# Kernel tuning notes

Measured on AMD Instinct MI355X. Metric: run time of the kernel, lower is better.

## Reference

```python
import jax, jax.numpy as jnp
import numpy as np

E = 64          # num_experts
D_IN = 512      # in_features
D_OUT = 512     # out_features
T = 262144      # total routed token-slots (grouped by expert, balanced)


def setup_inputs() -> dict:
    key = jax.random.key(0)
    k1, k2 = jax.random.split(key)
    STD = 0.02
    return {
        "input": jax.random.normal(k1, (T, D_IN), dtype=jnp.float32),
        # tokens are pre-grouped by expert; balanced routing -> equal counts
        "num_experts_per_token": jnp.full((E,), T // E, dtype=jnp.int64),
        "weight": jax.random.normal(k2, (E, D_OUT, D_IN), dtype=jnp.float32) * STD,
        "bias": jnp.zeros((E, D_OUT), dtype=jnp.float32),
    }


def reference(input, num_experts_per_token, weight, bias):
    # Faithful to the split + per-expert F.linear + cat path, for balanced
    # routing (equal counts per expert) so shapes are static under jit.
    e = weight.shape[0]
    tpe = input.shape[0] // e  # tokens per expert
    x = input.reshape(e, tpe, -1)                      # [E, tpe, D_in]
    # F.linear(x_e, W_e) = x_e @ W_e.T for each expert -> grouped GEMM
    out = jnp.einsum('eti,eoi->eto', x, weight)        # [E, tpe, D_out]
    out = out + bias[:, None, :]
    return out.reshape(e * tpe, -1)                    # [T, D_out]
```

## Files before the change

### kernel.cpp

```cpp
#include <hip/hip_runtime.h>
#include <hip/hip_bf16.h>


#define NEXPERT 64
#define DIN 512
#define DOUT 512
#define TPE 4096
#define BM 128
#define BN 256
#define BK 32
#define NKT (DIN / BK)

typedef __attribute__((ext_vector_type(8))) __bf16 bf16x8;
typedef __attribute__((ext_vector_type(4))) __bf16 bf16x4;
typedef __attribute__((ext_vector_type(4))) float f32x4;

__global__ __launch_bounds__(256)
void convert_w_kernel(const float* __restrict__ w, __bf16* __restrict__ wb) {
  size_t i = ((size_t)blockIdx.x * 256 + threadIdx.x) * 8;
  f32x4 a = *(const f32x4*)(w + i);
  f32x4 b = *(const f32x4*)(w + i + 4);
  bf16x8 r;
  r[0] = (__bf16)a[0]; r[1] = (__bf16)a[1]; r[2] = (__bf16)a[2]; r[3] = (__bf16)a[3];
  r[4] = (__bf16)b[0]; r[5] = (__bf16)b[1]; r[6] = (__bf16)b[2]; r[7] = (__bf16)b[3];
  *(bf16x8*)(wb + i) = r;
}

template <bool WB16>
__global__ __launch_bounds__(256, 2)
void moe_gemm(const float* __restrict__ x, const void* __restrict__ wsrc,
              const float* __restrict__ bias, float* __restrict__ out) {
  __shared__ __align__(16) unsigned char sA[2][BM * BK * 2];

  int bid = blockIdx.x;
  int swzb = (bid & 7) * 512 + (bid >> 3);
  int e  = swzb >> 6;
  int rr = swzb & 63;
  int mt = rr >> 1;
  int nt = rr & 1;

  const int tid  = threadIdx.x;
  const int lane = tid & 63;
  const int wn   = tid >> 6;
  const int r15  = lane & 15;
  const int kg   = lane >> 4;

  const int c4 = tid & 7;
  const int tr = tid >> 3;
  const float* aG = x + ((size_t)e * TPE + (size_t)mt * BM + tr) * DIN + c4 * 4;
  const int wrBase = tr * 64 + (((c4 >> 1) ^ ((tr >> 1) & 3)) << 4) + (c4 & 1) * 8;

  const int chz = (kg ^ ((r15 >> 1) & 3)) << 4;
  const int aRd = r15 * 64 + chz;

  const size_t bRow = (size_t)(e * DOUT + nt * BN + wn * 64 + r15) * DIN + kg * 8;
  const __bf16* bPb = (const __bf16*)wsrc + bRow;
  const float*  bPf = (const float*)wsrc + bRow;

  f32x4 sa0[4], sa1[4];
  bf16x8 b0v[4], b1v[4];

#define ISSUEA(kt, Sr)                                                      \
  { _Pragma("unroll") for (int i = 0; i < 4; ++i)                           \
      Sr[i] = *(const f32x4*)(aG + (size_t)i * 32 * DIN + (kt) * BK); }

#define WRITEA(dbuf, Sr)                                                    \
  { _Pragma("unroll") for (int i = 0; i < 4; ++i) {                         \
      bf16x4 c;                                                             \
      c[0] = (__bf16)Sr[i][0]; c[1] = (__bf16)Sr[i][1];                     \
      c[2] = (__bf16)Sr[i][2]; c[3] = (__bf16)Sr[i][3];                     \
      *(bf16x4*)(&sA[dbuf][wrBase + i * 2048]) = c; } }

#define LOADB(kt, Br)                                                       \
  { if constexpr (WB16) {                                                   \
      _Pragma("unroll") for (int n = 0; n < 4; ++n)                         \
        Br[n] = *(const bf16x8*)(bPb + (size_t)n * 16 * DIN + (kt) * BK);   \
    } else {                                                                \
      _Pragma("unroll") for (int n = 0; n < 4; ++n) {                       \
        f32x4 lo = *(const f32x4*)(bPf + (size_t)n * 16 * DIN + (kt) * BK); \
        f32x4 hi = *(const f32x4*)(bPf + (size_t)n * 16 * DIN + (kt) * BK + 4); \
        bf16x8 rv;                                                          \
        rv[0]=(__bf16)lo[0]; rv[1]=(__bf16)lo[1]; rv[2]=(__bf16)lo[2]; rv[3]=(__bf16)lo[3]; \
        rv[4]=(__bf16)hi[0]; rv[5]=(__bf16)hi[1]; rv[6]=(__bf16)hi[2]; rv[7]=(__bf16)hi[3]; \
        Br[n] = rv; } } }

#define MFMAS(Bv)                                                           \
  { _Pragma("unroll") for (int mi = 0; mi < 8; ++mi)                        \
      _Pragma("unroll") for (int ni = 0; ni < 4; ++ni)                      \
        acc[mi][ni] = __builtin_amdgcn_mfma_f32_16x16x32_bf16(              \
            af[mi], Bv[ni], acc[mi][ni], 0, 0, 0); }

  f32x4 acc[8][4];
#pragma unroll
  for (int m = 0; m < 8; ++m)
#pragma unroll
    for (int n = 0; n < 4; ++n) acc[m][n] = (f32x4)0.f;

  ISSUEA(0, sa0);
  ISSUEA(1, sa1);
  LOADB(0, b0v);
  WRITEA(0, sa0);
  asm volatile("s_waitcnt lgkmcnt(0)" ::: "memory");
  __builtin_amdgcn_s_barrier();

#pragma unroll
  for (int t = 0; t < NKT; ++t) {
    const int d = t & 1;
    bf16x8 af[8];
#pragma unroll
    for (int mi = 0; mi < 8; ++mi)
      af[mi] = *(const bf16x8*)(&sA[d][aRd + mi * 1024]);

    if (d == 0) {
      if (t + 1 < NKT) LOADB(t + 1, b1v);
      if (t + 2 < NKT) ISSUEA(t + 2, sa0);
      if (t + 1 < NKT) WRITEA(1, sa1);
      __builtin_amdgcn_s_setprio(1);
      MFMAS(b0v);
      __builtin_amdgcn_s_setprio(0);
    } else {
      if (t + 1 < NKT) LOADB(t + 1, b0v);
      if (t + 2 < NKT) ISSUEA(t + 2, sa1);
      if (t + 1 < NKT) WRITEA(0, sa0);
      __builtin_amdgcn_s_setprio(1);
      MFMAS(b1v);
      __builtin_amdgcn_s_setprio(0);
    }

    if (t + 1 < NKT) {
      asm volatile("s_waitcnt lgkmcnt(0)" ::: "memory");
      __builtin_amdgcn_s_barrier();
    }
  }

  float bv[4];
  const float* bp = bias + (size_t)e * DOUT + nt * BN + wn * 64 + r15;
#pragma unroll
  for (int n = 0; n < 4; ++n) bv[n] = bp[n * 16];

  const int q4 = (lane >> 4) * 4;
  float* Cb = out + ((size_t)e * TPE + (size_t)mt * BM) * DOUT + nt * BN + wn * 64;
#pragma unroll
  for (int m = 0; m < 8; ++m) {
#pragma unroll
    for (int j = 0; j < 4; ++j) {
      float* pr = Cb + (size_t)(m * 16 + q4 + j) * DOUT;
#pragma unroll
      for (int n = 0; n < 4; ++n)
        pr[n * 16 + r15] = acc[m][n][j] + bv[n];
    }
  }
#undef ISSUEA
#undef WRITEA
#undef LOADB
#undef MFMAS
}

extern "C" void kernel_launch(void* const* d_in, const int* in_sizes, int n_in,
                              void* d_out, int out_size, void* d_ws, size_t ws_size,
                              hipStream_t stream) {
  const float* x    = (const float*)d_in[0];
  const float* w    = (const float*)d_in[2];
  const float* bias = (const float*)d_in[3];
  float* out        = (float*)d_out;

  const size_t wElems = (size_t)NEXPERT * DOUT * DIN;
  const size_t needWs = wElems * sizeof(__hip_bfloat16);
  dim3 grid(NEXPERT * (TPE / BM) * (DOUT / BN));
  dim3 block(256);

  if (ws_size >= needWs) {
    dim3 cgrid(wElems / 8 / 256);
    hipLaunchKernelGGL(convert_w_kernel, cgrid, block, 0, stream,
                       w, (__bf16*)d_ws);
    hipLaunchKernelGGL(moe_gemm<true>, grid, block, 0, stream,
                       x, (const void*)d_ws, bias, out);
  } else {
    hipLaunchKernelGGL(moe_gemm<false>, grid, block, 0, stream,
                       x, (const void*)w, bias, out);
  }
}
```

Before: 339.6 us.

## Stage pre-packed bf16 weights into LDS via direct global-to-LDS loads

```diff
diff --git a/kernel.cpp b/kernel.cpp
--- a/kernel.cpp
+++ b/kernel.cpp
@@ -9,28 +9,36 @@
 #define BM 128
 #define BN 256
 #define BK 32
-#define NKT (DIN / BK)
+#define NKT 16
 
 typedef __attribute__((ext_vector_type(8))) __bf16 bf16x8;
 typedef __attribute__((ext_vector_type(4))) __bf16 bf16x4;
 typedef __attribute__((ext_vector_type(4))) float f32x4;
 
 __global__ __launch_bounds__(256)
-void convert_w_kernel(const float* __restrict__ w, __bf16* __restrict__ wb) {
-  size_t i = ((size_t)blockIdx.x * 256 + threadIdx.x) * 8;
-  f32x4 a = *(const f32x4*)(w + i);
-  f32x4 b = *(const f32x4*)(w + i + 4);
+void pack_w_kernel(const float* __restrict__ w, __bf16* __restrict__ wp) {
+  int S = blockIdx.x * 256 + threadIdx.x;
+  int l  = S & 63;
+  int c  = (S >> 6) & 15;
+  int kt = (S >> 10) & 15;
+  int nt = (S >> 14) & 1;
+  int e  = S >> 15;
+  int o  = nt * 256 + c * 16 + (l >> 2);
+  int kg = (l & 3) ^ ((l >> 3) & 3);
+  const float* src = w + ((size_t)(e * DOUT + o)) * DIN + kt * BK + kg * 8;
+  f32x4 lo = *(const f32x4*)(src);
+  f32x4 hi = *(const f32x4*)(src + 4);
   bf16x8 r;
-  r[0] = (__bf16)a[0]; r[1] = (__bf16)a[1]; r[2] = (__bf16)a[2]; r[3] = (__bf16)a[3];
-  r[4] = (__bf16)b[0]; r[5] = (__bf16)b[1]; r[6] = (__bf16)b[2]; r[7] = (__bf16)b[3];
-  *(bf16x8*)(wb + i) = r;
-}
-
-template <bool WB16>
+  r[0]=(__bf16)lo[0]; r[1]=(__bf16)lo[1]; r[2]=(__bf16)lo[2]; r[3]=(__bf16)lo[3];
+  r[4]=(__bf16)hi[0]; r[5]=(__bf16)hi[1]; r[6]=(__bf16)hi[2]; r[7]=(__bf16)hi[3];
+  *(bf16x8*)(wp + (size_t)S * 8) = r;
+}
+
 __global__ __launch_bounds__(256, 2)
-void moe_gemm(const float* __restrict__ x, const void* __restrict__ wsrc,
-              const float* __restrict__ bias, float* __restrict__ out) {
+void moe_gemm8(const float* __restrict__ x, const __bf16* __restrict__ wp,
+               const float* __restrict__ bias, float* __restrict__ out) {
   __shared__ __align__(16) unsigned char sA[2][BM * BK * 2];
+  __shared__ __align__(16) unsigned char sB[2][BN * BK * 2];
 
   int bid = blockIdx.x;
   int swzb = (bid & 7) * 512 + (bid >> 3);
@@ -52,43 +60,31 @@
 
   const int chz = (kg ^ ((r15 >> 1) & 3)) << 4;
   const int aRd = r15 * 64 + chz;
-
-  const size_t bRow = (size_t)(e * DOUT + nt * BN + wn * 64 + r15) * DIN + kg * 8;
-  const __bf16* bPb = (const __bf16*)wsrc + bRow;
-  const float*  bPf = (const float*)wsrc + bRow;
+  const int bRd = (wn * 64 + r15) * 64 + chz;
+
+  const __bf16* bSrc =
+      wp + ((size_t)(((e * 2 + nt) * 16) * 16 + wn * 4) * 64 + lane) * 8;
 
   f32x4 sa0[4], sa1[4];
-  bf16x8 b0v[4], b1v[4];
-
-#define ISSUEA(kt, Sr)                                                      \
-  { _Pragma("unroll") for (int i = 0; i < 4; ++i)                           \
+
+#define GLOADB(kt, dbuf)                                                     \
+  { _Pragma("unroll") for (int i = 0; i < 4; ++i)                            \
+      __builtin_amdgcn_global_load_lds(                                      \
+          (const __attribute__((address_space(1))) void*)(bSrc +             \
+              (size_t)(kt) * 8192 + i * 512),                                \
+          (__attribute__((address_space(3))) void*)(&sB[dbuf][(wn * 4 + i) * 1024]), \
+          16, 0, 0); }
+
+#define ISSUEA(kt, Sr)                                                       \
+  { _Pragma("unroll") for (int i = 0; i < 4; ++i)                            \
       Sr[i] = *(const f32x4*)(aG + (size_t)i * 32 * DIN + (kt) * BK); }
 
-#define WRITEA(dbuf, Sr)                                                    \
-  { _Pragma("unroll") for (int i = 0; i < 4; ++i) {                         \
-      bf16x4 c;                                                             \
-      c[0] = (__bf16)Sr[i][0]; c[1] = (__bf16)Sr[i][1];                     \
-      c[2] = (__bf16)Sr[i][2]; c[3] = (__bf16)Sr[i][3];                     \
-      *(bf16x4*)(&sA[dbuf][wrBase + i * 2048]) = c; } }
-
-#define LOADB(kt, Br)                                                       \
-  { if constexpr (WB16) {                                                   \
-      _Pragma("unroll") for (int n = 0; n < 4; ++n)                         \
-        Br[n] = *(const bf16x8*)(bPb + (size_t)n * 16 * DIN + (kt) * BK);   \
-    } else {                                                                \
-      _Pragma("unroll") for (int n = 0; n < 4; ++n) {                       \
-        f32x4 lo = *(const f32x4*)(bPf + (size_t)n * 16 * DIN + (kt) * BK); \
-        f32x4 hi = *(const f32x4*)(bPf + (size_t)n * 16 * DIN + (kt) * BK + 4); \
-        bf16x8 rv;                                                          \
-        rv[0]=(__bf16)lo[0]; rv[1]=(__bf16)lo[1]; rv[2]=(__bf16)lo[2]; rv[3]=(__bf16)lo[3]; \
-        rv[4]=(__bf16)hi[0]; rv[5]=(__bf16)hi[1]; rv[6]=(__bf16)hi[2]; rv[7]=(__bf16)hi[3]; \
-        Br[n] = rv; } } }
-
-#define MFMAS(Bv)                                                           \
-  { _Pragma("unroll") for (int mi = 0; mi < 8; ++mi)                        \
-      _Pragma("unroll") for (int ni = 0; ni < 4; ++ni)                      \
-        acc[mi][ni] = __builtin_amdgcn_mfma_f32_16x16x32_bf16(              \
-            af[mi], Bv[ni], acc[mi][ni], 0, 0, 0); }
+#define WRITEA(dbuf, Sr)                                                     \
+  { _Pragma("unroll") for (int i = 0; i < 4; ++i) {                          \
+      bf16x4 cc;                                                             \
+      cc[0] = (__bf16)Sr[i][0]; cc[1] = (__bf16)Sr[i][1];                    \
+      cc[2] = (__bf16)Sr[i][2]; cc[3] = (__bf16)Sr[i][3];                    \
+      *(bf16x4*)(&sA[dbuf][wrBase + i * 2048]) = cc; } }
 
   f32x4 acc[8][4];
 #pragma unroll
@@ -96,9 +92,9 @@
 #pragma unroll
     for (int n = 0; n < 4; ++n) acc[m][n] = (f32x4)0.f;
 
+  GLOADB(0, 0);
   ISSUEA(0, sa0);
   ISSUEA(1, sa1);
-  LOADB(0, b0v);
   WRITEA(0, sa0);
   asm volatile("s_waitcnt lgkmcnt(0)" ::: "memory");
   __builtin_amdgcn_s_barrier();
@@ -106,26 +102,47 @@
 #pragma unroll
   for (int t = 0; t < NKT; ++t) {
     const int d = t & 1;
-    bf16x8 af[8];
-#pragma unroll
-    for (int mi = 0; mi < 8; ++mi)
+    if (t == NKT - 1) {
+      asm volatile("s_waitcnt vmcnt(0)" ::: "memory");
+    } else {
+      asm volatile("s_waitcnt vmcnt(4)" ::: "memory");
+    }
+    if (t + 1 < NKT) GLOADB(t + 1, d ^ 1);
+    bf16x8 bfr[4], af[8];
+#pragma unroll
+    for (int ni = 0; ni < 4; ++ni)
+      bfr[ni] = *(const bf16x8*)(&sB[d][bRd + ni * 1024]);
+#pragma unroll
+    for (int mi = 0; mi < 4; ++mi)
       af[mi] = *(const bf16x8*)(&sA[d][aRd + mi * 1024]);
 
-    if (d == 0) {
-      if (t + 1 < NKT) LOADB(t + 1, b1v);
-      if (t + 2 < NKT) ISSUEA(t + 2, sa0);
-      if (t + 1 < NKT) WRITEA(1, sa1);
-      __builtin_amdgcn_s_setprio(1);
-      MFMAS(b0v);
-      __builtin_amdgcn_s_setprio(0);
-    } else {
-      if (t + 1 < NKT) LOADB(t + 1, b0v);
-      if (t + 2 < NKT) ISSUEA(t + 2, sa1);
-      if (t + 1 < NKT) WRITEA(0, sa0);
-      __builtin_amdgcn_s_setprio(1);
-      MFMAS(b1v);
-      __builtin_amdgcn_s_setprio(0);
-    }
+    if (t + 2 < NKT) {
+      if (d == 0) ISSUEA(t + 2, sa0) else ISSUEA(t + 2, sa1)
+    }
+    __builtin_amdgcn_s_setprio(1);
+#pragma unroll
+    for (int mi = 0; mi < 4; ++mi)
+#pragma unroll
+      for (int ni = 0; ni < 4; ++ni)
+        acc[mi][ni] = __builtin_amdgcn_mfma_f32_16x16x32_bf16(
+            af[mi], bfr[ni], acc[mi][ni], 0, 0, 0);
+    __builtin_amdgcn_s_setprio(0);
+
+#pragma unroll
+    for (int mi = 4; mi < 8; ++mi)
+      af[mi] = *(const bf16x8*)(&sA[d][aRd + mi * 1024]);
+    if (t + 1 < NKT) {
+      if (d == 0) WRITEA(1, sa1) else WRITEA(0, sa0)
+    }
+
+    __builtin_amdgcn_s_setprio(1);
+#pragma unroll
+    for (int mi = 4; mi < 8; ++mi)
+#pragma unroll
+      for (int ni = 0; ni < 4; ++ni)
+        acc[mi][ni] = __builtin_amdgcn_mfma_f32_16x16x32_bf16(
+            af[mi], bfr[ni], acc[mi][ni], 0, 0, 0);
+    __builtin_amdgcn_s_setprio(0);
 
     if (t + 1 < NKT) {
       asm volatile("s_waitcnt lgkmcnt(0)" ::: "memory");
@@ -150,10 +167,86 @@
         pr[n * 16 + r15] = acc[m][n][j] + bv[n];
     }
   }
+#undef GLOADB
 #undef ISSUEA
 #undef WRITEA
-#undef LOADB
-#undef MFMAS
+}
+
+typedef __attribute__((ext_vector_type(8))) __bf16 bf16x8_t;
+
+__device__ __forceinline__ bf16x8 cvt8f(f32x4 lo, f32x4 hi) {
+  bf16x8 r;
+  r[0]=(__bf16)lo[0]; r[1]=(__bf16)lo[1]; r[2]=(__bf16)lo[2]; r[3]=(__bf16)lo[3];
+  r[4]=(__bf16)hi[0]; r[5]=(__bf16)hi[1]; r[6]=(__bf16)hi[2]; r[7]=(__bf16)hi[3];
+  return r;
+}
+
+__global__ __launch_bounds__(256)
+void moe_fallback(const float* __restrict__ x, const float* __restrict__ w,
+                  const float* __restrict__ bias, float* __restrict__ out) {
+  __shared__ bf16x8 fA[2][512];
+  __shared__ bf16x8 fB[2][512];
+  int bid = blockIdx.x;
+  int swz = (bid & 7) * 1024 + (bid >> 3);
+  int e = swz >> 7, rr = swz & 127, mt = rr >> 2, nt = rr & 3;
+  const int t = threadIdx.x, lane = t & 63, wave = t >> 6;
+  const int wm = wave >> 1, wnn = wave & 1, r15 = lane & 15, kgf = lane >> 4;
+  const int rs = r15 * 4 + (kgf ^ ((r15 >> 1) & 3));
+  const int row0 = t >> 2, kg0 = t & 3;
+  const int slot0 = row0 * 4 + (kg0 ^ ((row0 >> 1) & 3));
+  const int slot1 = slot0 + 256;
+  const float* Ab = x + ((size_t)e * TPE + (size_t)mt * 128) * DIN;
+  const float* Bb = w + ((size_t)e * DOUT + (size_t)nt * 128) * DIN;
+  const int offA0 = row0 * DIN + kg0 * 8, offA1 = offA0 + 64 * DIN;
+  f32x4 a0l, a0h, a1l, a1h, b0l, b0h, b1l, b1h;
+  auto LOAD = [&](int kt) {
+    const float* pa0 = Ab + offA0 + kt * 32; const float* pa1 = Ab + offA1 + kt * 32;
+    const float* pb0 = Bb + offA0 + kt * 32; const float* pb1 = Bb + offA1 + kt * 32;
+    a0l = *(const f32x4*)(pa0); a0h = *(const f32x4*)(pa0 + 4);
+    a1l = *(const f32x4*)(pa1); a1h = *(const f32x4*)(pa1 + 4);
+    b0l = *(const f32x4*)(pb0); b0h = *(const f32x4*)(pb0 + 4);
+    b1l = *(const f32x4*)(pb1); b1h = *(const f32x4*)(pb1 + 4);
+  };
+  auto STORE = [&](int buf) {
+    fA[buf][slot0] = cvt8f(a0l, a0h); fA[buf][slot1] = cvt8f(a1l, a1h);
+    fB[buf][slot0] = cvt8f(b0l, b0h); fB[buf][slot1] = cvt8f(b1l, b1h);
+  };
+  f32x4 acc[4][4];
+#pragma unroll
+  for (int m = 0; m < 4; ++m)
+#pragma unroll
+    for (int n = 0; n < 4; ++n) acc[m][n] = (f32x4)0.f;
+  LOAD(0); STORE(0); __syncthreads();
+  int cur = 0;
+  for (int kt = 0; kt < NKT; ++kt) {
+    if (kt + 1 < NKT) LOAD(kt + 1);
+    bf16x8 af[4], bfr[4];
+#pragma unroll
+    for (int m = 0; m < 4; ++m) af[m] = fA[cur][wm * 256 + m * 64 + rs];
+#pragma unroll
+    for (int n = 0; n < 4; ++n) bfr[n] = fB[cur][wnn * 256 + n * 64 + rs];
+#pragma unroll
+    for (int m = 0; m < 4; ++m)
+#pragma unroll
+      for (int n = 0; n < 4; ++n)
+        acc[m][n] = __builtin_amdgcn_mfma_f32_16x16x32_bf16(af[m], bfr[n], acc[m][n], 0, 0, 0);
+    if (kt + 1 < NKT) { STORE(cur ^ 1); __syncthreads(); }
+    cur ^= 1;
+  }
+  float bv[4];
+  const float* bp = bias + (size_t)e * DOUT + nt * 128 + wnn * 64 + r15;
+#pragma unroll
+  for (int n = 0; n < 4; ++n) bv[n] = bp[n * 16];
+  const int q4 = (lane >> 4) * 4;
+  float* Cb = out + ((size_t)e * TPE + (size_t)mt * 128 + wm * 64) * DOUT + nt * 128 + wnn * 64;
+#pragma unroll
+  for (int m = 0; m < 4; ++m)
+#pragma unroll
+    for (int j = 0; j < 4; ++j) {
+      float* pr = Cb + (size_t)(m * 16 + q4 + j) * DOUT;
+#pragma unroll
+      for (int n = 0; n < 4; ++n) pr[n * 16 + r15] = acc[m][n][j] + bv[n];
+    }
 }
 
 extern "C" void kernel_launch(void* const* d_in, const int* in_sizes, int n_in,
@@ -166,17 +259,16 @@
 
   const size_t wElems = (size_t)NEXPERT * DOUT * DIN;
   const size_t needWs = wElems * sizeof(__hip_bfloat16);
-  dim3 grid(NEXPERT * (TPE / BM) * (DOUT / BN));
   dim3 block(256);
 
   if (ws_size >= needWs) {
-    dim3 cgrid(wElems / 8 / 256);
-    hipLaunchKernelGGL(convert_w_kernel, cgrid, block, 0, stream,
-                       w, (__bf16*)d_ws);
-    hipLaunchKernelGGL(moe_gemm<true>, grid, block, 0, stream,
-                       x, (const void*)d_ws, bias, out);
+    dim3 pgrid(wElems / 8 / 256);
+    hipLaunchKernelGGL(pack_w_kernel, pgrid, block, 0, stream, w, (__bf16*)d_ws);
+    dim3 grid(NEXPERT * (TPE / BM) * (DOUT / BN));
+    hipLaunchKernelGGL(moe_gemm8, grid, block, 0, stream,
+                       x, (const __bf16*)d_ws, bias, out);
   } else {
-    hipLaunchKernelGGL(moe_gemm<false>, grid, block, 0, stream,
-                       x, (const void*)w, bias, out);
-  }
-}
+    dim3 grid(NEXPERT * 32 * 4);
+    hipLaunchKernelGGL(moe_fallback, grid, block, 0, stream, x, w, bias, out);
+  }
+}
```

Measured after the change: 288.6 us. -15.0%, faster.
